# Optimization experiments

Hardware: AMD Instinct MI355X
Metric: run time of the kernel (lower is better)

Reference implementation:

```python
import jax, jax.numpy as jnp
import numpy as np
from jax import lax


def log_g(x):
    # log of g(x) = x + 0.5 for x >= 0, sigmoid(x) for x < 0
    return jnp.where(x >= 0, jnp.log(jax.nn.relu(x) + 0.5), -jax.nn.softplus(-x))


def setup_inputs() -> dict:
    key = jax.random.key(0)
    k1, k2, k3, k4 = jax.random.split(key, 4)
    N, L, H_in, H = 8, 4096, 1024, 1024
    x = jax.random.normal(k1, (N, L, H_in), dtype=jnp.float32)
    W = jax.random.normal(k2, (2 * H, H_in), dtype=jnp.float32) * (1.0 / np.sqrt(H_in))
    b = jax.random.normal(k3, (2 * H,), dtype=jnp.float32) * 0.01
    hx = jax.random.uniform(k4, (N, H), dtype=jnp.float32)  # positive initial state
    return {"x": x, "W": W, "b": b, "hx": hx}


def reference(x, W, b, hx):
    # linear_ih: (N, L, 2H)
    zh = jnp.einsum('nli,oi->nlo', x, W) + b
    z, h_inter = jnp.split(zh, 2, axis=-1)  # each (N, L, H)
    log_z = -jax.nn.softplus(-z)            # log sigmoid(z)
    log_coeffs = -jax.nn.softplus(z)        # log (1 - sigmoid(z))
    log_h0 = jnp.log(hx)[:, None, :]        # (N, 1, H)
    log_tilde_h = log_g(h_inter)
    log_values = jnp.concatenate([log_h0, log_z + log_tilde_h], axis=1)  # (N, L+1, H)
    # Heinsen parallel scan in log space
    a_star = jnp.pad(jnp.cumsum(log_coeffs, axis=1), ((0, 0), (1, 0), (0, 0)))  # (N, L+1, H)
    log_h = a_star + lax.cumlogsumexp(log_values - a_star, axis=1)
    h = jnp.exp(log_h)
    return h[:, 1:]  # (N, L, H)
```

## Files before the change

### kernel.cpp

```cpp
#include <hip/hip_runtime.h>
#include <hip/hip_bf16.h>
#include <hip/hip_fp16.h>


#define N_B   8
#define L_SEQ 4096
#define H_DIM 1024
#define K_DIM 1024
#define O_DIM 2048
#define M_TOT (N_B * L_SEQ)

#define BM 128
#define BN 128
#define BK 64

#define NCHUNK 128
#define CLEN   (L_SEQ / NCHUNK)
#define NCH    (N_B * H_DIM)

typedef unsigned short ushort_t;
typedef unsigned short us8 __attribute__((ext_vector_type(8)));
typedef __bf16 v8bf __attribute__((ext_vector_type(8)));
typedef float f32x4 __attribute__((ext_vector_type(4)));

static __device__ __forceinline__ ushort_t f2bf(float f) {
    __hip_bfloat16 h = __float2bfloat16(f);
    return *reinterpret_cast<ushort_t*>(&h);
}

static __device__ __forceinline__ void dma16(const ushort_t* g, ushort_t* l) {
    __builtin_amdgcn_global_load_lds(
        (const __attribute__((address_space(1))) unsigned int*)g,
        (__attribute__((address_space(3))) unsigned int*)l,
        16, 0, 0);
}

__global__ __launch_bounds__(256) void cvt_f32_bf16(
    const float* __restrict__ src, ushort_t* __restrict__ dst)
{
    const int i = blockIdx.x * 256 + threadIdx.x;
    const float4 f0 = ((const float4*)src)[2 * i];
    const float4 f1 = ((const float4*)src)[2 * i + 1];
    us8 o;
    o[0] = f2bf(f0.x); o[1] = f2bf(f0.y); o[2] = f2bf(f0.z); o[3] = f2bf(f0.w);
    o[4] = f2bf(f1.x); o[5] = f2bf(f1.y); o[6] = f2bf(f1.z); o[7] = f2bf(f1.w);
    ((us8*)dst)[i] = o;
}

__global__ __launch_bounds__(256) void gemm_zh(
    const ushort_t* __restrict__ Xb,
    const ushort_t* __restrict__ Wb,
    const float* __restrict__ bias,
    __half* __restrict__ zbuf,
    __half* __restrict__ hbuf)
{
    __shared__ ushort_t As[BM * BK];
    __shared__ ushort_t Bs[BN * BK];

    const int tid    = threadIdx.x;
    const int wave   = tid >> 6;
    const int lane   = tid & 63;
    const int lane15 = lane & 15;
    const int quad   = lane >> 4;

    const int n0 = blockIdx.x * BN;
    const int m0 = blockIdx.y * BM;

    const int lrow = lane >> 3;
    const int jj   = (lane & 7) ^ lrow;
    const ushort_t* gA = Xb + (size_t)(m0 + wave * 8 + lrow) * K_DIM + jj * 8;
    const ushort_t* gB = Wb + (size_t)(n0 + wave * 8 + lrow) * K_DIM + jj * 8;
    ushort_t* lA = &As[(wave * 8) * BK];
    ushort_t* lB = &Bs[(wave * 8) * BK];

    const int wm = (wave >> 1) * 64;
    const int wn = (wave & 1) * 64;

    int offA[2][4], offB[2][4];
#pragma unroll
    for (int s = 0; s < 2; ++s) {
#pragma unroll
        for (int t = 0; t < 4; ++t) {
            const int rowA = wm + t * 16 + lane15;
            offA[s][t] = rowA * BK + (((s * 4 + quad) ^ (rowA & 7)) * 8);
            const int rowB = wn + t * 16 + lane15;
            offB[s][t] = rowB * BK + (((s * 4 + quad) ^ (rowB & 7)) * 8);
        }
    }

    const f32x4 fzero = {0.f, 0.f, 0.f, 0.f};
    f32x4 acc[4][4];
#pragma unroll
    for (int i = 0; i < 4; ++i)
#pragma unroll
        for (int j = 0; j < 4; ++j)
            acc[i][j] = fzero;

    for (int kt = 0; kt < K_DIM / BK; ++kt) {
        __syncthreads();
#pragma unroll
        for (int r = 0; r < 4; ++r) {
            dma16(gA + (size_t)r * 32 * K_DIM + kt * BK, lA + r * 32 * BK);
            dma16(gB + (size_t)r * 32 * K_DIM + kt * BK, lB + r * 32 * BK);
        }
        __syncthreads();

#pragma unroll
        for (int s = 0; s < 2; ++s) {
            v8bf af[4], bfr[4];
#pragma unroll
            for (int t = 0; t < 4; ++t) af[t]  = *(const v8bf*)(&As[offA[s][t]]);
#pragma unroll
            for (int t = 0; t < 4; ++t) bfr[t] = *(const v8bf*)(&Bs[offB[s][t]]);
#pragma unroll
            for (int i = 0; i < 4; ++i)
#pragma unroll
                for (int j = 0; j < 4; ++j)
                    acc[i][j] = __builtin_amdgcn_mfma_f32_16x16x32_bf16(
                        af[i], bfr[j], acc[i][j], 0, 0, 0);
        }
    }

    float bv[4];
#pragma unroll
    for (int j = 0; j < 4; ++j)
        bv[j] = bias[n0 + wn + j * 16 + lane15];

    __half* outb = (n0 < H_DIM) ? zbuf : hbuf;
    const int colbase = (n0 & (H_DIM - 1)) + wn + lane15;

#pragma unroll
    for (int i = 0; i < 4; ++i) {
#pragma unroll
        for (int r = 0; r < 4; ++r) {
            const size_t row = (size_t)(m0 + wm + i * 16 + quad * 4 + r);
            __half* p = outb + row * H_DIM + colbase;
#pragma unroll
            for (int j = 0; j < 4; ++j)
                p[j * 16] = __float2half(acc[i][j][r] + bv[j]);
        }
    }
}

__device__ __forceinline__ void gate_av(float z, float hi, float& a, float& v)
{
    const float e  = __expf(-z);
    const float sz = 1.0f / (1.0f + e);
    a = e * sz;
    const float g = (hi >= 0.0f) ? (hi + 0.5f)
                                 : (1.0f / (1.0f + __expf(-hi)));
    v = sz * g;
}

__global__ __launch_bounds__(256) void scan_phase1(
    const __half* __restrict__ zbuf, const __half* __restrict__ hbuf,
    float* __restrict__ Aar, float* __restrict__ Bar)
{
    const int idx = blockIdx.x * 256 + threadIdx.x;
    const int h4  = (idx & 255) << 2;
    const int n   = (idx >> 8) & 7;
    const int c   = idx >> 11;
    const size_t base = ((size_t)(n * L_SEQ + c * CLEN)) * H_DIM + h4;
    const float2* zp = (const float2*)(zbuf + base);
    const float2* hp = (const float2*)(hbuf + base);

    float A[4], B[4];
#pragma unroll
    for (int j = 0; j < 4; ++j) { A[j] = 1.f; B[j] = 0.f; }

#pragma unroll 8
    for (int s = 0; s < CLEN; ++s) {
        float2 zr = zp[(size_t)s * (H_DIM / 4)];
        float2 hr = hp[(size_t)s * (H_DIM / 4)];
        const __half2* z2 = (const __half2*)&zr;
        const __half2* i2 = (const __half2*)&hr;
#pragma unroll
        for (int j = 0; j < 2; ++j) {
            const float2 z  = __half22float2(z2[j]);
            const float2 hi = __half22float2(i2[j]);
            float a, v;
            gate_av(z.x, hi.x, a, v);
            B[2*j]   = fmaf(a, B[2*j],   v);  A[2*j]   *= a;
            gate_av(z.y, hi.y, a, v);
            B[2*j+1] = fmaf(a, B[2*j+1], v);  A[2*j+1] *= a;
        }
    }
    const size_t o = (size_t)c * NCH + n * H_DIM + h4;
    *(f32x4*)(Aar + o) = *(const f32x4*)&A[0];
    *(f32x4*)(Bar + o) = *(const f32x4*)&B[0];
}

__global__ __launch_bounds__(256) void scan_phase2(
    const float* __restrict__ Aar, const float* __restrict__ Bar,
    const float* __restrict__ hx, float* __restrict__ seed)
{
    const int ch = blockIdx.x * 256 + threadIdx.x;
    float carry = hx[ch];
#pragma unroll 8
    for (int c = 0; c < NCHUNK; ++c) {
        seed[c * NCH + ch] = carry;
        carry = fmaf(Aar[c * NCH + ch], carry, Bar[c * NCH + ch]);
    }
}

__global__ __launch_bounds__(256) void scan_phase3(
    const __half* __restrict__ zbuf, const __half* __restrict__ hbuf,
    const float* __restrict__ seed, float* __restrict__ out)
{
    const int idx = blockIdx.x * 256 + threadIdx.x;
    const int h4  = (idx & 255) << 2;
    const int n   = (idx >> 8) & 7;
    const int c   = idx >> 11;
    const size_t base = ((size_t)(n * L_SEQ + c * CLEN)) * H_DIM + h4;
    const float2* zp = (const float2*)(zbuf + base);
    const float2* hp = (const float2*)(hbuf + base);
    float* op = out + base;

    const size_t so = (size_t)c * NCH + n * H_DIM + h4;
    float h0[4];
    *(f32x4*)h0 = *(const f32x4*)(seed + so);

#pragma unroll 8
    for (int s = 0; s < CLEN; ++s) {
        float2 zr = zp[(size_t)s * (H_DIM / 4)];
        float2 hr = hp[(size_t)s * (H_DIM / 4)];
        const __half2* z2 = (const __half2*)&zr;
        const __half2* i2 = (const __half2*)&hr;
#pragma unroll
        for (int j = 0; j < 2; ++j) {
            const float2 za = __half22float2(z2[j]);
            const float2 ia = __half22float2(i2[j]);
            float a, v;
            gate_av(za.x, ia.x, a, v);  h0[2*j]   = fmaf(a, h0[2*j],   v);
            gate_av(za.y, ia.y, a, v);  h0[2*j+1] = fmaf(a, h0[2*j+1], v);
        }
        f32x4 hv = *(const f32x4*)h0;
        __builtin_nontemporal_store(hv, (f32x4*)(op + (size_t)s * H_DIM));
    }
}

extern "C" void kernel_launch(void* const* d_in, const int* in_sizes, int n_in,
                              void* d_out, int out_size, void* d_ws, size_t ws_size,
                              hipStream_t stream)
{
    const float* X    = (const float*)d_in[0];
    const float* Wm   = (const float*)d_in[1];
    const float* bias = (const float*)d_in[2];
    const float* hx   = (const float*)d_in[3];
    float* out = (float*)d_out;

    char* ws = (char*)d_ws;
    ushort_t* wb = (ushort_t*)ws;
    __half* zbuf = (__half*)(ws + (size_t)O_DIM * K_DIM * 2);
    __half* hbuf = zbuf + (size_t)M_TOT * H_DIM;
    float*  seed = (float*)(hbuf + (size_t)M_TOT * H_DIM);

    ushort_t* xb = (ushort_t*)d_out;
    float* Aar = out + (size_t)M_TOT * H_DIM / 2;
    float* Bar = Aar + (size_t)NCHUNK * NCH;

    cvt_f32_bf16<<<O_DIM * K_DIM / 8 / 256, 256, 0, stream>>>(Wm, wb);
    cvt_f32_bf16<<<M_TOT * K_DIM / 8 / 256, 256, 0, stream>>>(X, xb);

    dim3 ggrid(O_DIM / BN, M_TOT / BM);
    gemm_zh<<<ggrid, 256, 0, stream>>>(xb, wb, bias, zbuf, hbuf);

    const int p13_blocks = (NCH / 4) * NCHUNK / 256;
    scan_phase1<<<p13_blocks, 256, 0, stream>>>(zbuf, hbuf, Aar, Bar);
    scan_phase2<<<NCH / 256, 256, 0, stream>>>(Aar, Bar, hx, seed);
    scan_phase3<<<p13_blocks, 256, 0, stream>>>(zbuf, hbuf, seed, out);
}
```

Baseline: 459.7 us.

## Rewrite GEMM as 256x256 double-buffered tile with 8 waves and XCD swizzle

The bf16 GEMM tile grows from 128x128 to 256x256 with 512 threads (8 waves, each computing 128x64). LDS is double-buffered so the global-to-LDS DMA for tile k+2 overlaps the MFMA work on tile k, using explicit vmcnt waits and barriers. MFMA sections run at raised wave priority, and a workgroup index remap spreads neighbouring tiles across XCDs for L2 reuse. The cost is higher register and LDS pressure (128 KB LDS per block, two blocks per CU requested) and more intricate hand-written synchronisation.

```diff
diff --git a/kernel.cpp b/kernel.cpp
--- a/kernel.cpp
+++ b/kernel.cpp
@@ -10,9 +10,10 @@
 #define O_DIM 2048
 #define M_TOT (N_B * L_SEQ)
 
-#define BM 128
-#define BN 128
+#define BM 256
+#define BN 256
 #define BK 64
+#define KTILES (K_DIM / BK)
 
 #define NCHUNK 128
 #define CLEN   (L_SEQ / NCHUNK)
@@ -47,93 +48,140 @@
     ((us8*)dst)[i] = o;
 }
 
-__global__ __launch_bounds__(256) void gemm_zh(
+__global__ __launch_bounds__(512, 2) void gemm_zh(
     const ushort_t* __restrict__ Xb,
     const ushort_t* __restrict__ Wb,
     const float* __restrict__ bias,
     __half* __restrict__ zbuf,
     __half* __restrict__ hbuf)
 {
-    __shared__ ushort_t As[BM * BK];
-    __shared__ ushort_t Bs[BN * BK];
-
-    const int tid    = threadIdx.x;
-    const int wave   = tid >> 6;
-    const int lane   = tid & 63;
-    const int lane15 = lane & 15;
-    const int quad   = lane >> 4;
-
-    const int n0 = blockIdx.x * BN;
-    const int m0 = blockIdx.y * BM;
-
-    const int lrow = lane >> 3;
-    const int jj   = (lane & 7) ^ lrow;
-    const ushort_t* gA = Xb + (size_t)(m0 + wave * 8 + lrow) * K_DIM + jj * 8;
-    const ushort_t* gB = Wb + (size_t)(n0 + wave * 8 + lrow) * K_DIM + jj * 8;
-    ushort_t* lA = &As[(wave * 8) * BK];
-    ushort_t* lB = &Bs[(wave * 8) * BK];
-
-    const int wm = (wave >> 1) * 64;
-    const int wn = (wave & 1) * 64;
-
-    int offA[2][4], offB[2][4];
-#pragma unroll
-    for (int s = 0; s < 2; ++s) {
-#pragma unroll
-        for (int t = 0; t < 4; ++t) {
-            const int rowA = wm + t * 16 + lane15;
-            offA[s][t] = rowA * BK + (((s * 4 + quad) ^ (rowA & 7)) * 8);
-            const int rowB = wn + t * 16 + lane15;
-            offB[s][t] = rowB * BK + (((s * 4 + quad) ^ (rowB & 7)) * 8);
-        }
-    }
+    __shared__ ushort_t As[2][BM * BK];
+    __shared__ ushort_t Bs[2][BN * BK];
+
+    const int tid  = threadIdx.x;
+    const int wave = tid >> 6;
+    const int lane = tid & 63;
+    const int l15  = lane & 15;
+    const int quad = lane >> 4;
+    const int wr   = wave >> 2;
+    const int wc   = wave & 3;
+
+    const int orig = blockIdx.x;
+    const int wg   = (orig & 7) * (1024 / 8) + (orig >> 3);
+    const int n0   = (wg & 7) * BN;
+    const int m0   = (wg >> 3) * BM;
+
+    const int lrow3  = lane >> 3;
+    const int colofs = ((lane & 7) ^ lrow3) * 8;
+    const ushort_t* gA = Xb + (size_t)(m0 + wave * 8 + lrow3) * K_DIM + colofs;
+    const ushort_t* gB = Wb + (size_t)(n0 + wave * 8 + lrow3) * K_DIM + colofs;
+    const int ldst = wave * 512;
+
+#define STAGE(kt, b) do {                                                     \
+        const size_t ko_ = (size_t)(kt) * BK;                                 \
+        _Pragma("unroll")                                                     \
+        for (int h_ = 0; h_ < 2; ++h_) {                                      \
+            _Pragma("unroll")                                                 \
+            for (int l_ = 0; l_ < 2; ++l_) {                                  \
+                const size_t gofs_ = (size_t)(h_ * 128 + l_ * 64) * K_DIM;    \
+                const int lofs_ = h_ * 8192 + l_ * 4096 + ldst;               \
+                dma16(gA + gofs_ + ko_, &As[b][lofs_]);                       \
+                dma16(gB + gofs_ + ko_, &Bs[b][lofs_]);                       \
+            }                                                                 \
+        }                                                                     \
+    } while (0)
+
+    int xt[2];
+#pragma unroll
+    for (int s = 0; s < 2; ++s) xt[s] = (((s * 4 + quad) ^ (l15 & 7)) * 8);
+    const int arow0 = (wr * 128 + l15) * BK;
+    const int brow0 = (wc * 64 + l15) * BK;
 
     const f32x4 fzero = {0.f, 0.f, 0.f, 0.f};
-    f32x4 acc[4][4];
-#pragma unroll
-    for (int i = 0; i < 4; ++i)
+    f32x4 acc[8][4];
+#pragma unroll
+    for (int i = 0; i < 8; ++i)
 #pragma unroll
         for (int j = 0; j < 4; ++j)
             acc[i][j] = fzero;
 
-    for (int kt = 0; kt < K_DIM / BK; ++kt) {
-        __syncthreads();
+    v8bf bfr[4][2];
+
+    STAGE(0, 0);
+    STAGE(1, 1);
+    asm volatile("s_waitcnt vmcnt(8)" ::: "memory");
+    __builtin_amdgcn_s_barrier();
+    asm volatile("" ::: "memory");
+
+    for (int kt = 0; kt < KTILES; ++kt) {
+        const int b = kt & 1;
+
+#pragma unroll
+        for (int p = 0; p < 4; ++p) {
+            if (p == 0) {
+#pragma unroll
+                for (int j = 0; j < 4; ++j)
+#pragma unroll
+                    for (int s = 0; s < 2; ++s)
+                        bfr[j][s] = *(const v8bf*)&Bs[b][brow0 + j * 16 * BK + xt[s]];
+            }
+            v8bf af[2][2];
+#pragma unroll
+            for (int u = 0; u < 2; ++u)
+#pragma unroll
+                for (int s = 0; s < 2; ++s)
+                    af[u][s] = *(const v8bf*)&As[b][arow0 + (2 * p + u) * 16 * BK + xt[s]];
+
+            asm volatile("" ::: "memory");
+            __builtin_amdgcn_s_barrier();
+
+            __builtin_amdgcn_s_setprio(1);
+#pragma unroll
+            for (int s = 0; s < 2; ++s)
+#pragma unroll
+                for (int u = 0; u < 2; ++u)
+#pragma unroll
+                    for (int j = 0; j < 4; ++j)
+                        acc[2 * p + u][j] = __builtin_amdgcn_mfma_f32_16x16x32_bf16(
+                            af[u][s], bfr[j][s], acc[2 * p + u][j], 0, 0, 0);
+            __builtin_amdgcn_s_setprio(0);
+
+            if (p < 3) {
+                asm volatile("" ::: "memory");
+                __builtin_amdgcn_s_barrier();
+                asm volatile("" ::: "memory");
+            }
+        }
+
+        if (kt < KTILES - 1) {
+            asm volatile("" ::: "memory");
+            __builtin_amdgcn_s_barrier();
+            asm volatile("" ::: "memory");
+            if (kt + 2 < KTILES) {
+                STAGE(kt + 2, b);
+                asm volatile("s_waitcnt vmcnt(8)" ::: "memory");
+            } else {
+                asm volatile("s_waitcnt vmcnt(0)" ::: "memory");
+            }
+            __builtin_amdgcn_s_barrier();
+            asm volatile("" ::: "memory");
+        }
+    }
+#undef STAGE
+
+    float bv[4];
+#pragma unroll
+    for (int j = 0; j < 4; ++j)
+        bv[j] = bias[n0 + wc * 64 + j * 16 + l15];
+
+    __half* outb = (n0 < H_DIM) ? zbuf : hbuf;
+    const int colbase = (n0 & (H_DIM - 1)) + wc * 64 + l15;
+
+#pragma unroll
+    for (int i = 0; i < 8; ++i) {
 #pragma unroll
         for (int r = 0; r < 4; ++r) {
-            dma16(gA + (size_t)r * 32 * K_DIM + kt * BK, lA + r * 32 * BK);
-            dma16(gB + (size_t)r * 32 * K_DIM + kt * BK, lB + r * 32 * BK);
-        }
-        __syncthreads();
-
-#pragma unroll
-        for (int s = 0; s < 2; ++s) {
-            v8bf af[4], bfr[4];
-#pragma unroll
-            for (int t = 0; t < 4; ++t) af[t]  = *(const v8bf*)(&As[offA[s][t]]);
-#pragma unroll
-            for (int t = 0; t < 4; ++t) bfr[t] = *(const v8bf*)(&Bs[offB[s][t]]);
-#pragma unroll
-            for (int i = 0; i < 4; ++i)
-#pragma unroll
-                for (int j = 0; j < 4; ++j)
-                    acc[i][j] = __builtin_amdgcn_mfma_f32_16x16x32_bf16(
-                        af[i], bfr[j], acc[i][j], 0, 0, 0);
-        }
-    }
-
-    float bv[4];
-#pragma unroll
-    for (int j = 0; j < 4; ++j)
-        bv[j] = bias[n0 + wn + j * 16 + lane15];
-
-    __half* outb = (n0 < H_DIM) ? zbuf : hbuf;
-    const int colbase = (n0 & (H_DIM - 1)) + wn + lane15;
-
-#pragma unroll
-    for (int i = 0; i < 4; ++i) {
-#pragma unroll
-        for (int r = 0; r < 4; ++r) {
-            const size_t row = (size_t)(m0 + wm + i * 16 + quad * 4 + r);
+            const size_t row = (size_t)(m0 + wr * 128 + i * 16 + quad * 4 + r);
             __half* p = outb + row * H_DIM + colbase;
 #pragma unroll
             for (int j = 0; j < 4; ++j)
@@ -262,8 +310,8 @@
     cvt_f32_bf16<<<O_DIM * K_DIM / 8 / 256, 256, 0, stream>>>(Wm, wb);
     cvt_f32_bf16<<<M_TOT * K_DIM / 8 / 256, 256, 0, stream>>>(X, xb);
 
-    dim3 ggrid(O_DIM / BN, M_TOT / BM);
-    gemm_zh<<<ggrid, 256, 0, stream>>>(xb, wb, bias, zbuf, hbuf);
+    const int ggrid = (O_DIM / BN) * (M_TOT / BM);
+    gemm_zh<<<ggrid, 512, 0, stream>>>(xb, wb, bias, zbuf, hbuf);
 
     const int p13_blocks = (NCH / 4) * NCHUNK / 256;
     scan_phase1<<<p13_blocks, 256, 0, stream>>>(zbuf, hbuf, Aar, Bar);
```

After: 475.0 us. +3.3%, slower.

## Fuse gate computation and chunk-local scan reduction into GEMM epilogue

Applied to the files above, without the earlier changes.

Permutes W and bias rows so each GEMM tile holds interleaved z/h column pairs. The epilogue can then compute the gate coefficients (a, v), store them as packed half2, and reduce per-32-row chunk carry pairs (A, B) with wave shuffles. This removes the separate scan_phase1 kernel, which re-read both fp16 intermediates, and lets phase3 skip recomputing the gates. The costs are extra epilogue work and register pressure in the GEMM, two small permutation kernels, and fp16 rounding of a and v, with the chunk products computed from the rounded values to stay consistent.

```diff
diff --git a/kernel.cpp b/kernel.cpp
--- a/kernel.cpp
+++ b/kernel.cpp
@@ -47,12 +47,47 @@
     ((us8*)dst)[i] = o;
 }
 
+__global__ __launch_bounds__(256) void cvt_w_perm(
+    const float* __restrict__ src, ushort_t* __restrict__ dst)
+{
+    const int i  = blockIdx.x * 256 + threadIdx.x;
+    const int op = i >> 7;
+    const int k  = (i & 127) * 8;
+    const int B  = op >> 4, t = op & 15;
+    const int orig = (B & 1) * 1024 + (B >> 1) * 16 + t;
+    const float4* s = (const float4*)(src + (size_t)orig * K_DIM + k);
+    const float4 f0 = s[0], f1 = s[1];
+    us8 o;
+    o[0] = f2bf(f0.x); o[1] = f2bf(f0.y); o[2] = f2bf(f0.z); o[3] = f2bf(f0.w);
+    o[4] = f2bf(f1.x); o[5] = f2bf(f1.y); o[6] = f2bf(f1.z); o[7] = f2bf(f1.w);
+    *(us8*)(dst + (size_t)op * K_DIM + k) = o;
+}
+
+__global__ __launch_bounds__(256) void bias_perm(
+    const float* __restrict__ b, float* __restrict__ bp)
+{
+    const int i = blockIdx.x * 256 + threadIdx.x;
+    const int B = i >> 4, t = i & 15;
+    bp[i] = b[(B & 1) * 1024 + (B >> 1) * 16 + t];
+}
+
+__device__ __forceinline__ void gate_av(float z, float hi, float& a, float& v)
+{
+    const float e  = __expf(-z);
+    const float sz = 1.0f / (1.0f + e);
+    a = e * sz;
+    const float g = (hi >= 0.0f) ? (hi + 0.5f)
+                                 : (1.0f / (1.0f + __expf(-hi)));
+    v = sz * g;
+}
+
 __global__ __launch_bounds__(256) void gemm_zh(
     const ushort_t* __restrict__ Xb,
     const ushort_t* __restrict__ Wb,
-    const float* __restrict__ bias,
-    __half* __restrict__ zbuf,
-    __half* __restrict__ hbuf)
+    const float* __restrict__ biasp,
+    __half2* __restrict__ avbuf,
+    float* __restrict__ Aar,
+    float* __restrict__ Bar)
 {
     __shared__ ushort_t As[BM * BK];
     __shared__ ushort_t Bs[BN * BK];
@@ -124,70 +159,64 @@
     float bv[4];
 #pragma unroll
     for (int j = 0; j < 4; ++j)
-        bv[j] = bias[n0 + wn + j * 16 + lane15];
-
-    __half* outb = (n0 < H_DIM) ? zbuf : hbuf;
-    const int colbase = (n0 & (H_DIM - 1)) + wn + lane15;
+        bv[j] = biasp[n0 + wn + j * 16 + lane15];
+
+    const int chbase = ((n0 + wn) >> 1) + lane15;
+
+    float Ai[4][2], Bi[4][2];
 
 #pragma unroll
     for (int i = 0; i < 4; ++i) {
+        float A[2] = {1.f, 1.f};
+        float Bc[2] = {0.f, 0.f};
 #pragma unroll
         for (int r = 0; r < 4; ++r) {
             const size_t row = (size_t)(m0 + wm + i * 16 + quad * 4 + r);
-            __half* p = outb + row * H_DIM + colbase;
-#pragma unroll
-            for (int j = 0; j < 4; ++j)
-                p[j * 16] = __float2half(acc[i][j][r] + bv[j]);
-        }
-    }
-}
-
-__device__ __forceinline__ void gate_av(float z, float hi, float& a, float& v)
-{
-    const float e  = __expf(-z);
-    const float sz = 1.0f / (1.0f + e);
-    a = e * sz;
-    const float g = (hi >= 0.0f) ? (hi + 0.5f)
-                                 : (1.0f / (1.0f + __expf(-hi)));
-    v = sz * g;
-}
-
-__global__ __launch_bounds__(256) void scan_phase1(
-    const __half* __restrict__ zbuf, const __half* __restrict__ hbuf,
-    float* __restrict__ Aar, float* __restrict__ Bar)
-{
-    const int idx = blockIdx.x * 256 + threadIdx.x;
-    const int h4  = (idx & 255) << 2;
-    const int n   = (idx >> 8) & 7;
-    const int c   = idx >> 11;
-    const size_t base = ((size_t)(n * L_SEQ + c * CLEN)) * H_DIM + h4;
-    const float2* zp = (const float2*)(zbuf + base);
-    const float2* hp = (const float2*)(hbuf + base);
-
-    float A[4], B[4];
-#pragma unroll
-    for (int j = 0; j < 4; ++j) { A[j] = 1.f; B[j] = 0.f; }
-
-#pragma unroll 8
-    for (int s = 0; s < CLEN; ++s) {
-        float2 zr = zp[(size_t)s * (H_DIM / 4)];
-        float2 hr = hp[(size_t)s * (H_DIM / 4)];
-        const __half2* z2 = (const __half2*)&zr;
-        const __half2* i2 = (const __half2*)&hr;
-#pragma unroll
-        for (int j = 0; j < 2; ++j) {
-            const float2 z  = __half22float2(z2[j]);
-            const float2 hi = __half22float2(i2[j]);
-            float a, v;
-            gate_av(z.x, hi.x, a, v);
-            B[2*j]   = fmaf(a, B[2*j],   v);  A[2*j]   *= a;
-            gate_av(z.y, hi.y, a, v);
-            B[2*j+1] = fmaf(a, B[2*j+1], v);  A[2*j+1] *= a;
-        }
-    }
-    const size_t o = (size_t)c * NCH + n * H_DIM + h4;
-    *(f32x4*)(Aar + o) = *(const f32x4*)&A[0];
-    *(f32x4*)(Bar + o) = *(const f32x4*)&B[0];
+            __half2* prow = avbuf + row * H_DIM + chbase;
+#pragma unroll
+            for (int jp = 0; jp < 2; ++jp) {
+                const float z  = acc[i][2 * jp][r]     + bv[2 * jp];
+                const float hh = acc[i][2 * jp + 1][r] + bv[2 * jp + 1];
+                float a, v;
+                gate_av(z, hh, a, v);
+                const __half2 h2 = __floats2half2_rn(a, v);
+                prow[jp * 16] = h2;
+                const float2 f = __half22float2(h2);
+                Bc[jp] = fmaf(f.x, Bc[jp], f.y);
+                A[jp] *= f.x;
+            }
+        }
+#pragma unroll
+        for (int jp = 0; jp < 2; ++jp) {
+#pragma unroll
+            for (int d = 16; d < 64; d <<= 1) {
+                const float Ay = __shfl_xor(A[jp],  d);
+                const float By = __shfl_xor(Bc[jp], d);
+                Bc[jp] = (lane & d) ? fmaf(A[jp], By, Bc[jp])
+                                    : fmaf(Ay, Bc[jp], By);
+                A[jp] *= Ay;
+            }
+            Ai[i][jp] = A[jp];
+            Bi[i][jp] = Bc[jp];
+        }
+    }
+
+    if (lane < 16) {
+#pragma unroll
+        for (int cc = 0; cc < 2; ++cc) {
+            const int grow = m0 + wm + cc * 32;
+            const int n    = grow >> 12;
+            const int cch  = (grow & (L_SEQ - 1)) >> 5;
+            const size_t o = (size_t)cch * NCH + (size_t)n * H_DIM + chbase;
+#pragma unroll
+            for (int jp = 0; jp < 2; ++jp) {
+                const float A0 = Ai[2 * cc][jp],     B0 = Bi[2 * cc][jp];
+                const float A1 = Ai[2 * cc + 1][jp], B1 = Bi[2 * cc + 1][jp];
+                Aar[o + jp * 16] = A1 * A0;
+                Bar[o + jp * 16] = fmaf(A1, B0, B1);
+            }
+        }
+    }
 }
 
 __global__ __launch_bounds__(256) void scan_phase2(
@@ -204,7 +233,7 @@
 }
 
 __global__ __launch_bounds__(256) void scan_phase3(
-    const __half* __restrict__ zbuf, const __half* __restrict__ hbuf,
+    const __half2* __restrict__ avbuf,
     const float* __restrict__ seed, float* __restrict__ out)
 {
     const int idx = blockIdx.x * 256 + threadIdx.x;
@@ -212,8 +241,7 @@
     const int n   = (idx >> 8) & 7;
     const int c   = idx >> 11;
     const size_t base = ((size_t)(n * L_SEQ + c * CLEN)) * H_DIM + h4;
-    const float2* zp = (const float2*)(zbuf + base);
-    const float2* hp = (const float2*)(hbuf + base);
+    const float4* avp = (const float4*)(avbuf + base);
     float* op = out + base;
 
     const size_t so = (size_t)c * NCH + n * H_DIM + h4;
@@ -222,17 +250,12 @@
 
 #pragma unroll 8
     for (int s = 0; s < CLEN; ++s) {
-        float2 zr = zp[(size_t)s * (H_DIM / 4)];
-        float2 hr = hp[(size_t)s * (H_DIM / 4)];
-        const __half2* z2 = (const __half2*)&zr;
-        const __half2* i2 = (const __half2*)&hr;
-#pragma unroll
-        for (int j = 0; j < 2; ++j) {
-            const float2 za = __half22float2(z2[j]);
-            const float2 ia = __half22float2(i2[j]);
-            float a, v;
-            gate_av(za.x, ia.x, a, v);  h0[2*j]   = fmaf(a, h0[2*j],   v);
-            gate_av(za.y, ia.y, a, v);  h0[2*j+1] = fmaf(a, h0[2*j+1], v);
+        float4 avr = avp[(size_t)s * (H_DIM / 4)];
+        const __half2* a2 = (const __half2*)&avr;
+#pragma unroll
+        for (int j = 0; j < 4; ++j) {
+            const float2 av = __half22float2(a2[j]);
+            h0[j] = fmaf(av.x, h0[j], av.y);
         }
         f32x4 hv = *(const f32x4*)h0;
         __builtin_nontemporal_store(hv, (f32x4*)(op + (size_t)s * H_DIM));
@@ -250,23 +273,24 @@
     float* out = (float*)d_out;
 
     char* ws = (char*)d_ws;
-    ushort_t* wb = (ushort_t*)ws;
-    __half* zbuf = (__half*)(ws + (size_t)O_DIM * K_DIM * 2);
-    __half* hbuf = zbuf + (size_t)M_TOT * H_DIM;
-    float*  seed = (float*)(hbuf + (size_t)M_TOT * H_DIM);
+    ushort_t* wb   = (ushort_t*)ws;
+    __half2*  avbuf = (__half2*)(ws + (size_t)O_DIM * K_DIM * 2);
+    float*    seed = (float*)((char*)avbuf + (size_t)M_TOT * H_DIM * 4);
+    float*    biasp = seed + (size_t)NCHUNK * NCH;
 
     ushort_t* xb = (ushort_t*)d_out;
     float* Aar = out + (size_t)M_TOT * H_DIM / 2;
     float* Bar = Aar + (size_t)NCHUNK * NCH;
 
-    cvt_f32_bf16<<<O_DIM * K_DIM / 8 / 256, 256, 0, stream>>>(Wm, wb);
+    cvt_w_perm<<<O_DIM * K_DIM / 8 / 256, 256, 0, stream>>>(Wm, wb);
+    bias_perm<<<O_DIM / 256, 256, 0, stream>>>(bias, biasp);
     cvt_f32_bf16<<<M_TOT * K_DIM / 8 / 256, 256, 0, stream>>>(X, xb);
 
     dim3 ggrid(O_DIM / BN, M_TOT / BM);
-    gemm_zh<<<ggrid, 256, 0, stream>>>(xb, wb, bias, zbuf, hbuf);
-
-    const int p13_blocks = (NCH / 4) * NCHUNK / 256;
-    scan_phase1<<<p13_blocks, 256, 0, stream>>>(zbuf, hbuf, Aar, Bar);
+    gemm_zh<<<ggrid, 256, 0, stream>>>(xb, wb, biasp, avbuf, Aar, Bar);
+
     scan_phase2<<<NCH / 256, 256, 0, stream>>>(Aar, Bar, hx, seed);
-    scan_phase3<<<p13_blocks, 256, 0, stream>>>(zbuf, hbuf, seed, out);
-}
+
+    const int p3_blocks = (NCH / 4) * NCHUNK / 256;
+    scan_phase3<<<p3_blocks, 256, 0, stream>>>(avbuf, seed, out);
+}
```

Result: faster. 443.5 us (-3.5%).
